# Performance work log

Hardware: AMD Instinct MI355X
Metric: run time of the kernel (lower is better)

Reference implementation:

```python
import jax, jax.numpy as jnp
import numpy as np

THRESH = 0.85

def setup_inputs() -> dict:
    key = jax.random.key(0)
    k1, k2 = jax.random.split(key)
    bs, d, r, c = 4, 16, 64, 64
    n = r * c
    seg = jax.random.normal(k1, (bs, d, r, c), dtype=jnp.float32)
    W = jax.random.uniform(k2, (bs, n, n), dtype=jnp.float32)
    return {"seg": seg, "W": W}

def reference(seg, W):
    bs, d, r, c = seg.shape
    # threshold affinity: keep values > 0.85
    Wt = jnp.where(W > THRESH, W, jnp.zeros((), W.dtype))
    # row-normalize: D = diag(1/rowsum(Wt)) @ Wt  (broadcast division)
    D = Wt / Wt.sum(axis=-1, keepdims=True)          # [bs, n, n]
    seg_flat = seg.reshape(bs, d, r * c)             # [bs, d, n]
    # seg_flat @ D^T : out[b,d,m] = sum_n seg[b,d,n] * D[b,m,n]
    out = jnp.einsum('bdn,bmn->bdm', seg_flat, D)
    return out.reshape(bs, d, r, c)
```

## Files before the change

### kernel.cpp

```cpp
#include <hip/hip_runtime.h>


#define N_DIM 4096
#define D_DIM 16
#define THRESH 0.85f
#define ROWS_PER_WAVE 4

__global__ __launch_bounds__(256) void regu_kernel(
    const float* __restrict__ seg,
    const float* __restrict__ W,
    float* __restrict__ out)
{
    const int lane = threadIdx.x & 63;
    const int wave_in_block = threadIdx.x >> 6;
    const int gwave = blockIdx.x * 4 + wave_in_block;
    const int row_base = gwave * ROWS_PER_WAVE;
    const int b  = row_base >> 12;
    const int m0 = row_base & (N_DIM - 1);

    const float* Wp   = W   + ((size_t)b * N_DIM + m0) * N_DIM;
    const float* segp = seg + (size_t)b * D_DIM * N_DIM;

    float acc[ROWS_PER_WAVE][D_DIM];
    float rowsum[ROWS_PER_WAVE];
#pragma unroll
    for (int r = 0; r < ROWS_PER_WAVE; ++r) {
        rowsum[r] = 0.0f;
#pragma unroll
        for (int d = 0; d < D_DIM; ++d) acc[r][d] = 0.0f;
    }

    for (int n0 = 0; n0 < N_DIM; n0 += 256) {
        const int idx = n0 + lane * 4;

        float4 w4[ROWS_PER_WAVE];
#pragma unroll
        for (int r = 0; r < ROWS_PER_WAVE; ++r) {
            float4 v = *(const float4*)(Wp + (size_t)r * N_DIM + idx);
            v.x = (v.x > THRESH) ? v.x : 0.0f;
            v.y = (v.y > THRESH) ? v.y : 0.0f;
            v.z = (v.z > THRESH) ? v.z : 0.0f;
            v.w = (v.w > THRESH) ? v.w : 0.0f;
            w4[r] = v;
            rowsum[r] += (v.x + v.y) + (v.z + v.w);
        }

#pragma unroll
        for (int d = 0; d < D_DIM; ++d) {
            const float4 s = *(const float4*)(segp + d * N_DIM + idx);
#pragma unroll
            for (int r = 0; r < ROWS_PER_WAVE; ++r) {
                acc[r][d] += w4[r].x * s.x;
                acc[r][d] += w4[r].y * s.y;
                acc[r][d] += w4[r].z * s.z;
                acc[r][d] += w4[r].w * s.w;
            }
        }
    }

#pragma unroll
    for (int r = 0; r < ROWS_PER_WAVE; ++r) {
#pragma unroll
        for (int d = 0; d < D_DIM; ++d) {
            float v = acc[r][d];
#pragma unroll
            for (int off = 1; off < 64; off <<= 1) v += __shfl_xor(v, off, 64);
            acc[r][d] = v;
        }
        float s = rowsum[r];
#pragma unroll
        for (int off = 1; off < 64; off <<= 1) s += __shfl_xor(s, off, 64);
        rowsum[r] = s;
    }

    if (lane == 0) {
#pragma unroll
        for (int r = 0; r < ROWS_PER_WAVE; ++r) {
            const float inv = 1.0f / rowsum[r];
#pragma unroll
            for (int d = 0; d < D_DIM; ++d) {
                out[((size_t)b * D_DIM + d) * N_DIM + (m0 + r)] = acc[r][d] * inv;
            }
        }
    }
}

extern "C" void kernel_launch(void* const* d_in, const int* in_sizes, int n_in,
                              void* d_out, int out_size, void* d_ws, size_t ws_size,
                              hipStream_t stream) {
    const float* seg = (const float*)d_in[0];
    const float* W   = (const float*)d_in[1];
    float* out = (float*)d_out;

    regu_kernel<<<1024, 256, 0, stream>>>(seg, W, out);
}
```

Baseline: 384.0 us.

## Double-buffer W loads and use recursive-halving transpose reduction across lanes

W row chunks are now prefetched into registers one chunk ahead, so global loads overlap the FMA work. The 64 per-lane partial sums are reduced with a butterfly scheme that halves the value count at each shuffle step, replacing 64 independent 6-step shuffle reductions. Each lane ends up holding one output, so all 64 lanes write instead of only lane 0. Launch bounds now request occupancy, which may constrain registers given the extra prefetch buffers.

```diff
diff --git a/kernel.cpp b/kernel.cpp
--- a/kernel.cpp
+++ b/kernel.cpp
@@ -4,9 +4,10 @@
 #define N_DIM 4096
 #define D_DIM 16
 #define THRESH 0.85f
-#define ROWS_PER_WAVE 4
+#define RPW 4
+#define CHUNK 256
 
-__global__ __launch_bounds__(256) void regu_kernel(
+__global__ __launch_bounds__(256, 4) void regu_kernel(
     const float* __restrict__ seg,
     const float* __restrict__ W,
     float* __restrict__ out)
@@ -14,29 +15,31 @@
     const int lane = threadIdx.x & 63;
     const int wave_in_block = threadIdx.x >> 6;
     const int gwave = blockIdx.x * 4 + wave_in_block;
-    const int row_base = gwave * ROWS_PER_WAVE;
+    const int row_base = gwave * RPW;
     const int b  = row_base >> 12;
     const int m0 = row_base & (N_DIM - 1);
 
-    const float* Wp   = W   + ((size_t)b * N_DIM + m0) * N_DIM;
-    const float* segp = seg + (size_t)b * D_DIM * N_DIM;
+    const float* Wp   = W   + ((size_t)b * N_DIM + m0) * N_DIM + lane * 4;
+    const float* segp = seg + (size_t)b * D_DIM * N_DIM + lane * 4;
 
-    float acc[ROWS_PER_WAVE][D_DIM];
-    float rowsum[ROWS_PER_WAVE];
+    float vals[64];
+    float rowsum[RPW];
 #pragma unroll
-    for (int r = 0; r < ROWS_PER_WAVE; ++r) {
-        rowsum[r] = 0.0f;
+    for (int i = 0; i < 64; ++i) vals[i] = 0.0f;
 #pragma unroll
-        for (int d = 0; d < D_DIM; ++d) acc[r][d] = 0.0f;
-    }
+    for (int r = 0; r < RPW; ++r) rowsum[r] = 0.0f;
 
-    for (int n0 = 0; n0 < N_DIM; n0 += 256) {
-        const int idx = n0 + lane * 4;
+    float4 wbuf0[RPW], wbuf1[RPW];
 
-        float4 w4[ROWS_PER_WAVE];
 #pragma unroll
-        for (int r = 0; r < ROWS_PER_WAVE; ++r) {
-            float4 v = *(const float4*)(Wp + (size_t)r * N_DIM + idx);
+    for (int r = 0; r < RPW; ++r)
+        wbuf0[r] = *(const float4*)(Wp + (size_t)r * N_DIM);
+
+    auto compute = [&](const float4* wsrc, int c) {
+        float4 w4[RPW];
+#pragma unroll
+        for (int r = 0; r < RPW; ++r) {
+            float4 v = wsrc[r];
             v.x = (v.x > THRESH) ? v.x : 0.0f;
             v.y = (v.y > THRESH) ? v.y : 0.0f;
             v.z = (v.z > THRESH) ? v.z : 0.0f;
@@ -44,45 +47,64 @@
             w4[r] = v;
             rowsum[r] += (v.x + v.y) + (v.z + v.w);
         }
+        const float* sp = segp + c * CHUNK;
+#pragma unroll
+        for (int d = 0; d < D_DIM; ++d) {
+            const float4 s = *(const float4*)(sp + d * N_DIM);
+#pragma unroll
+            for (int r = 0; r < RPW; ++r) {
+                vals[r * D_DIM + d] += w4[r].x * s.x;
+                vals[r * D_DIM + d] += w4[r].y * s.y;
+                vals[r * D_DIM + d] += w4[r].z * s.z;
+                vals[r * D_DIM + d] += w4[r].w * s.w;
+            }
+        }
+    };
+
+    for (int c = 0; c < N_DIM / CHUNK; c += 2) {
+        {
+            const float* p = Wp + (size_t)(c + 1) * CHUNK;
+#pragma unroll
+            for (int r = 0; r < RPW; ++r)
+                wbuf1[r] = *(const float4*)(p + (size_t)r * N_DIM);
+        }
+        compute(wbuf0, c);
+
+        if (c + 2 < N_DIM / CHUNK) {
+            const float* p = Wp + (size_t)(c + 2) * CHUNK;
+#pragma unroll
+            for (int r = 0; r < RPW; ++r)
+                wbuf0[r] = *(const float4*)(p + (size_t)r * N_DIM);
+        }
+        compute(wbuf1, c + 1);
+    }
 
 #pragma unroll
-        for (int d = 0; d < D_DIM; ++d) {
-            const float4 s = *(const float4*)(segp + d * N_DIM + idx);
+    for (int k = 0; k < 6; ++k) {
+        const int S = 32 >> k;
+        const bool up = (lane >> k) & 1;
 #pragma unroll
-            for (int r = 0; r < ROWS_PER_WAVE; ++r) {
-                acc[r][d] += w4[r].x * s.x;
-                acc[r][d] += w4[r].y * s.y;
-                acc[r][d] += w4[r].z * s.z;
-                acc[r][d] += w4[r].w * s.w;
-            }
+        for (int j = 0; j < S; ++j) {
+            const float mine = up ? vals[j + S] : vals[j];
+            const float send = up ? vals[j] : vals[j + S];
+            vals[j] = mine + __shfl_xor(send, 1 << k, 64);
         }
     }
 
 #pragma unroll
-    for (int r = 0; r < ROWS_PER_WAVE; ++r) {
-#pragma unroll
-        for (int d = 0; d < D_DIM; ++d) {
-            float v = acc[r][d];
-#pragma unroll
-            for (int off = 1; off < 64; off <<= 1) v += __shfl_xor(v, off, 64);
-            acc[r][d] = v;
-        }
+    for (int r = 0; r < RPW; ++r) {
         float s = rowsum[r];
 #pragma unroll
         for (int off = 1; off < 64; off <<= 1) s += __shfl_xor(s, off, 64);
         rowsum[r] = s;
     }
 
-    if (lane == 0) {
-#pragma unroll
-        for (int r = 0; r < ROWS_PER_WAVE; ++r) {
-            const float inv = 1.0f / rowsum[r];
-#pragma unroll
-            for (int d = 0; d < D_DIM; ++d) {
-                out[((size_t)b * D_DIM + d) * N_DIM + (m0 + r)] = acc[r][d] * inv;
-            }
-        }
-    }
+    const int j = __brev((unsigned)lane) >> 26;
+    const int r = j >> 4;
+    const int d = j & 15;
+    const float inv = 1.0f / (r < 2 ? (r == 0 ? rowsum[0] : rowsum[1])
+                                    : (r == 2 ? rowsum[2] : rowsum[3]));
+    out[((size_t)b * D_DIM + d) * N_DIM + (m0 + r)] = vals[0] * inv;
 }
 
 extern "C" void kernel_launch(void* const* d_in, const int* in_sizes, int n_in,
```

Measured after the change: 685.7 us. 78.6% more time.
